# Performance work log

Hardware: AMD Instinct MI355X
Metric: run time of the kernel (lower is better)

The kernel has to match this reference:

```python
import jax, jax.numpy as jnp
import numpy as np

B, N, ND, H, FF, L, NH = 8, 200, 128, 256, 1024, 3, 8
DH = H // NH


def setup_inputs() -> dict:
    key = jax.random.key(0)
    ks = jax.random.split(key, 16)
    w = lambda k, s: jax.random.normal(k, s, jnp.float32) * 0.02
    return dict(
        h=jax.random.normal(ks[0], (B, N, ND), jnp.float32),
        xt=jax.random.uniform(ks[1], (B, N, N), jnp.float32),
        t=jax.random.uniform(ks[2], (B,), jnp.float32),
        tw1=w(ks[3], (1, H)), tb1=jnp.zeros(H), tw2=w(ks[4], (H, H)), tb2=jnp.zeros(H),
        ew=w(ks[5], (1, H)), eb=jnp.zeros(H),
        pw=w(ks[6], (ND, H)), pb=jnp.zeros(H),
        qkv_w=w(ks[7], (L, H, 3 * H)), qkv_b=jnp.zeros((L, 3 * H)),
        ao_w=w(ks[8], (L, H, H)), ao_b=jnp.zeros((L, H)),
        ln1_g=jnp.ones((L, H)), ln1_b=jnp.zeros((L, H)),
        f1_w=w(ks[9], (L, H, FF)), f1_b=jnp.zeros((L, FF)),
        f2_w=w(ks[10], (L, FF, H)), f2_b=jnp.zeros((L, H)),
        ln2_g=jnp.ones((L, H)), ln2_b=jnp.zeros((L, H)),
        ow1=w(ks[11], (3 * H, H)), ob1=jnp.zeros(H),
        ow2=w(ks[12], (H, 2)), ob2=jnp.zeros(2),
    )


def _ln(x, g, b, eps=1e-5):
    m = x.mean(-1, keepdims=True)
    v = x.var(-1, keepdims=True)
    return (x - m) / jnp.sqrt(v + eps) * g + b


def _forward(h, xt, t, tw1, tb1, tw2, tb2, ew, eb, pw, pb,
             qkv_w, qkv_b, ao_w, ao_b, ln1_g, ln1_b,
             f1_w, f1_b, f2_w, f2_b, ln2_g, ln2_b, ow1, ob1, ow2, ob2):
    b, n, _ = h.shape
    # time embedding: Linear -> SiLU -> Linear
    t_emb = jax.nn.silu(t[:, None] @ tw1 + tb1) @ tw2 + tb2          # (B,H)
    x = h @ pw + pb + t_emb[:, None, :]                               # (B,N,H)
    # post-norm TransformerEncoderLayer stack (ReLU FFN, eval mode)
    for l in range(L):
        qkv = x @ qkv_w[l] + qkv_b[l]
        q, k, v = jnp.split(qkv, 3, axis=-1)
        q = q.reshape(b, n, NH, DH)
        k = k.reshape(b, n, NH, DH)
        v = v.reshape(b, n, NH, DH)
        scores = jnp.einsum('bihd,bjhd->bhij', q, k) / np.sqrt(DH).astype(np.float32)
        attn = jax.nn.softmax(scores, axis=-1)
        o = jnp.einsum('bhij,bjhd->bihd', attn, v).reshape(b, n, H)
        o = o @ ao_w[l] + ao_b[l]
        x = _ln(x + o, ln1_g[l], ln1_b[l])
        f = jax.nn.relu(x @ f1_w[l] + f1_b[l]) @ f2_w[l] + f2_b[l]
        x = _ln(x + f, ln2_g[l], ln2_b[l])
    # edge head: concat([h_i, h_j, edge_emb]) @ W1 == sum of three partial matmuls
    edge_emb = xt[..., None] * ew[0] + eb                             # (B,N,N,H)
    wa, wb, wc = ow1[:H], ow1[H:2 * H], ow1[2 * H:]
    pre = (x @ wa)[:, :, None, :] + (x @ wb)[:, None, :, :] \
        + edge_emb @ wc + ob1                                         # (B,N,N,H)
    return jax.nn.silu(pre) @ ow2 + ob2                               # (B,N,N,2)


def reference(h, xt, t, tw1, tb1, tw2, tb2, ew, eb, pw, pb,
              qkv_w, qkv_b, ao_w, ao_b, ln1_g, ln1_b,
              f1_w, f1_b, f2_w, f2_b, ln2_g, ln2_b, ow1, ob1, ow2, ob2):
    return _forward(h, xt, t, tw1, tb1, tw2, tb2, ew, eb, pw, pb,
                    qkv_w, qkv_b, ao_w, ao_b, ln1_g, ln1_b,
                    f1_w, f1_b, f2_w, f2_b, ln2_g, ln2_b, ow1, ob1, ow2, ob2)
```

## Files before the change

### kernel.cpp

```cpp
#include <hip/hip_runtime.h>

#define Bdim 8
#define Nn 200
#define NDd 128
#define Hd 256
#define FFd 1024
#define Ld 3
#define NHh 8
#define DHd 32
#define Mtot (Bdim * Nn)
#define ZS 409600

typedef unsigned short u16;
typedef unsigned int u32;
using short8 = __attribute__((ext_vector_type(8))) short;
using fx4 = __attribute__((ext_vector_type(4))) float;

__device__ __forceinline__ float siluf(float x) {
  return x * __builtin_amdgcn_rcpf(1.0f + __expf(-x));
}

__device__ __forceinline__ void bsplit(float x, u16& h, u16& l) {
  u32 b = __float_as_uint(x);
  h = (u16)(b >> 16);
  float hf = __uint_as_float(b & 0xffff0000u);
  float r = x - hf;
  l = (u16)(__float_as_uint(r) >> 16);
}

__device__ __forceinline__ void store_xfrag(u16* __restrict__ xh,
                                            u16* __restrict__ xl, int m, int c,
                                            float v) {
  u32 o = ((u32)((m >> 4) * 8 + (c >> 5)) * 64 + ((c & 31) >> 3) * 16 +
           (m & 15)) * 8 + (c & 7);
  u16 hh, ll;
  bsplit(v, hh, ll);
  xh[o] = hh;
  xl[o] = ll;
}

struct SplitDesc {
  const float* s;
  u32 off;
  int K, N;
};
struct SplitArgs {
  SplitDesc d[14];
};

__global__ __launch_bounds__(256) void prep_kernel(
    SplitArgs a, u16* __restrict__ WH, u16* __restrict__ WL,
    const float* __restrict__ t, const float* __restrict__ tw1,
    const float* __restrict__ tb1, const float* __restrict__ tw2,
    const float* __restrict__ tb2, float* __restrict__ temb,
    const float* __restrict__ ew, const float* __restrict__ eb,
    const float* __restrict__ ow1, const float* __restrict__ ob1,
    float* __restrict__ u, float* __restrict__ w0) {
  __shared__ float s[Hd];
  if (blockIdx.y < 14) {
    SplitDesc dd = a.d[blockIdx.y];
    int idx = blockIdx.x * 256 + threadIdx.x;
    int total8 = dd.K * dd.N / 8;
    if (idx >= total8) return;
    int n = idx % dd.N;
    int kq = idx / dd.N;
    int ks = kq >> 2, q = kq & 3;
    int KS = dd.K >> 5;
    short8 vh, vl;
#pragma unroll
    for (int kr = 0; kr < 8; ++kr) {
      float v = dd.s[(size_t)(ks * 32 + q * 8 + kr) * dd.N + n];
      u16 hh, ll;
      bsplit(v, hh, ll);
      vh[kr] = (short)hh;
      vl[kr] = (short)ll;
    }
    u32 o = (((u32)(n >> 4) * KS + ks) * 64 + q * 16 + (n & 15)) * 8 + dd.off;
    *(short8*)(WH + o) = vh;
    *(short8*)(WL + o) = vl;
  } else {
    if (blockIdx.x < 8) {
      int b = blockIdx.x, h = threadIdx.x;
      float pre = t[b] * tw1[h] + tb1[h];
      s[h] = siluf(pre);
      __syncthreads();
      float acc = tb2[h];
#pragma unroll 8
      for (int k = 0; k < Hd; ++k) acc += s[k] * tw2[k * Hd + h];
      temb[b * Hd + h] = acc;
    } else if (blockIdx.x == 8) {
      int c = threadIdx.x;
      const float* wcp = ow1 + 2 * Hd * Hd;
      float uu = 0.f, ww = 0.f;
      for (int hh = 0; hh < Hd; ++hh) {
        float wv = wcp[hh * Hd + c];
        uu += ew[hh] * wv;
        ww += eb[hh] * wv;
      }
      u[c] = uu;
      w0[c] = ww + ob1[c];
    }
  }
}

__global__ __launch_bounds__(256) void proj_kernel(
    const float* __restrict__ h, const float* __restrict__ pw,
    const float* __restrict__ pb, const float* __restrict__ temb,
    float* __restrict__ x, u16* __restrict__ xh, u16* __restrict__ xl) {
  int m = blockIdx.x, n = threadIdx.x, b = m / Nn;
  __shared__ float hs[NDd];
  if (n < NDd) hs[n] = h[m * NDd + n];
  __syncthreads();
  float acc = pb[n] + temb[b * Hd + n];
#pragma unroll 8
  for (int k = 0; k < NDd; ++k) acc += hs[k] * pw[k * Hd + n];
  x[m * Hd + n] = acc;
  store_xfrag(xh, xl, m, n, acc);
}

template <int KSZ, int EPI, int MERGE>
__global__ __launch_bounds__(256) void mfma_gemm(
    const u16* __restrict__ ah, const u16* __restrict__ al,
    const float* __restrict__ pO, const float* __restrict__ pl,
    const u16* __restrict__ wh, const u16* __restrict__ wl,
    const float* __restrict__ bias, float* __restrict__ outf,
    u16* __restrict__ oh, u16* __restrict__ ol, int N, int KS,
    size_t zstride) {
  int lane = threadIdx.x & 63, wv = threadIdx.x >> 6;
  int rt = blockIdx.x * 4 + wv;
  int nt0 = blockIdx.y * 4;
  int ks0 = blockIdx.z * KSZ;
  int m16 = lane & 15, quad = lane >> 4;
  int mrow = rt * 16 + m16;
  int bq = mrow / Nn, iq = mrow % Nn;
  fx4 z4 = {0.f, 0.f, 0.f, 0.f};
  fx4 acc[4] = {z4, z4, z4, z4};
  const short8* pah = (const short8*)ah;
  const short8* pal = (const short8*)al;
  const short8* pwh = (const short8*)wh;
  const short8* pwl = (const short8*)wl;

  auto loadA = [&](int ks, short8& a_h, short8& a_l) {
    if (MERGE) {
      int head = ks0 + ks;
      float o8[8];
      float denom = 0.f;
#pragma unroll
      for (int z = 0; z < 4; ++z) {
        int base = ((bq * NHh + head) * 4 + z) * Nn + iq;
        denom += pl[base];
        const float* p = pO + (size_t)base * 32 + quad * 8;
        float4 v0 = *(const float4*)p;
        float4 v1 = *(const float4*)(p + 4);
        if (z == 0) {
          o8[0] = v0.x; o8[1] = v0.y; o8[2] = v0.z; o8[3] = v0.w;
          o8[4] = v1.x; o8[5] = v1.y; o8[6] = v1.z; o8[7] = v1.w;
        } else {
          o8[0] += v0.x; o8[1] += v0.y; o8[2] += v0.z; o8[3] += v0.w;
          o8[4] += v1.x; o8[5] += v1.y; o8[6] += v1.z; o8[7] += v1.w;
        }
      }
      float rd = 1.0f / denom;
#pragma unroll
      for (int e = 0; e < 8; ++e) {
        u16 hh, ll;
        bsplit(o8[e] * rd, hh, ll);
        a_h[e] = (short)hh;
        a_l[e] = (short)ll;
      }
    } else {
      a_h = pah[(size_t)(rt * KS + ks0 + ks) * 64 + lane];
      a_l = pal[(size_t)(rt * KS + ks0 + ks) * 64 + lane];
    }
  };

  short8 ca_h, ca_l, cb_h[4], cb_l[4];
  loadA(0, ca_h, ca_l);
#pragma unroll
  for (int nt = 0; nt < 4; ++nt) {
    size_t wi = ((size_t)(nt0 + nt) * KS + ks0) * 64 + lane;
    cb_h[nt] = pwh[wi];
    cb_l[nt] = pwl[wi];
  }
#pragma unroll
  for (int ks = 0; ks < KSZ; ++ks) {
    short8 na_h, na_l, nb_h[4], nb_l[4];
    if (ks + 1 < KSZ) {
      loadA(ks + 1, na_h, na_l);
#pragma unroll
      for (int nt = 0; nt < 4; ++nt) {
        size_t wi = ((size_t)(nt0 + nt) * KS + ks0 + ks + 1) * 64 + lane;
        nb_h[nt] = pwh[wi];
        nb_l[nt] = pwl[wi];
      }
    }
#pragma unroll
    for (int nt = 0; nt < 4; ++nt) {
      acc[nt] = __builtin_amdgcn_mfma_f32_16x16x32_bf16(ca_h, cb_h[nt], acc[nt], 0, 0, 0);
      acc[nt] = __builtin_amdgcn_mfma_f32_16x16x32_bf16(ca_h, cb_l[nt], acc[nt], 0, 0, 0);
      acc[nt] = __builtin_amdgcn_mfma_f32_16x16x32_bf16(ca_l, cb_h[nt], acc[nt], 0, 0, 0);
    }
    ca_h = na_h;
    ca_l = na_l;
#pragma unroll
    for (int nt = 0; nt < 4; ++nt) {
      cb_h[nt] = nb_h[nt];
      cb_l[nt] = nb_l[nt];
    }
  }

  size_t zoff = (size_t)blockIdx.z * zstride;
#pragma unroll
  for (int nt = 0; nt < 4; ++nt) {
    int col = (nt0 + nt) * 16 + m16;
    float bv = (bias && blockIdx.z == 0) ? bias[col] : 0.f;
#pragma unroll
    for (int r = 0; r < 4; ++r) {
      int row = rt * 16 + quad * 4 + r;
      float v = acc[nt][r] + bv;
      if (EPI == 0) {
        outf[zoff + (size_t)row * N + col] = v;
      } else {
        v = fmaxf(v, 0.f);
        u32 o = ((u32)(rt * 32 + (col >> 5)) * 64 + ((col & 31) >> 3) * 16 +
                 (row & 15)) * 8 + (col & 7);
        u16 hh, ll;
        bsplit(v, hh, ll);
        oh[o] = hh;
        ol[o] = ll;
      }
    }
  }
}

__global__ __launch_bounds__(256) void afbm_gemm(
    const u16* __restrict__ xh, const u16* __restrict__ xl,
    const u16* __restrict__ WHa, const u16* __restrict__ WLa,
    const u16* __restrict__ WHb, const u16* __restrict__ WLb,
    const float* __restrict__ w0, float* __restrict__ Af,
    float* __restrict__ Bm) {
  int lane = threadIdx.x & 63, wv = threadIdx.x >> 6;
  int rt = blockIdx.x * 4 + wv;
  int sel = blockIdx.y >> 2;
  int nt0 = (blockIdx.y & 3) * 4;
  const short8* pwh = (const short8*)(sel ? WHb : WHa);
  const short8* pwl = (const short8*)(sel ? WLb : WLa);
  float* outp = sel ? Bm : Af;
  fx4 z4 = {0.f, 0.f, 0.f, 0.f};
  fx4 acc[4] = {z4, z4, z4, z4};
  const short8* pah = (const short8*)xh + (size_t)(rt * 8) * 64 + lane;
  const short8* pal = (const short8*)xl + (size_t)(rt * 8) * 64 + lane;
#pragma unroll 4
  for (int ks = 0; ks < 8; ++ks) {
    short8 a_h = pah[ks * 64];
    short8 a_l = pal[ks * 64];
#pragma unroll
    for (int nt = 0; nt < 4; ++nt) {
      size_t wi = ((size_t)(nt0 + nt) * 8 + ks) * 64 + lane;
      short8 b_h = pwh[wi];
      short8 b_l = pwl[wi];
      acc[nt] = __builtin_amdgcn_mfma_f32_16x16x32_bf16(a_h, b_h, acc[nt], 0, 0, 0);
      acc[nt] = __builtin_amdgcn_mfma_f32_16x16x32_bf16(a_h, b_l, acc[nt], 0, 0, 0);
      acc[nt] = __builtin_amdgcn_mfma_f32_16x16x32_bf16(a_l, b_h, acc[nt], 0, 0, 0);
    }
  }
  int q = lane >> 4, n16 = lane & 15;
#pragma unroll
  for (int nt = 0; nt < 4; ++nt) {
    int col = (nt0 + nt) * 16 + n16;
    float bv = (sel == 0) ? w0[col] : 0.f;
#pragma unroll
    for (int r = 0; r < 4; ++r) {
      int row = rt * 16 + q * 4 + r;
      outp[(size_t)row * Hd + col] = acc[nt][r] + bv;
    }
  }
}

__global__ __launch_bounds__(256) void ln_res_kernel(
    float* __restrict__ x, const float* __restrict__ y, int ksplit,
    const float* __restrict__ bias, const float* __restrict__ g,
    const float* __restrict__ bb, u16* __restrict__ xh, u16* __restrict__ xl) {
  int m = blockIdx.x, tid = threadIdx.x;
  int lane = tid & 63, wid = tid >> 6;
  float v = x[m * Hd + tid] + bias[tid];
  for (int z = 0; z < ksplit; ++z)
    v += y[(size_t)z * ZS + m * Hd + tid];
  float s = v, s2 = v * v;
  for (int off = 32; off; off >>= 1) {
    s += __shfl_down(s, off);
    s2 += __shfl_down(s2, off);
  }
  __shared__ float ps[4], ps2[4];
  if (!lane) { ps[wid] = s; ps2[wid] = s2; }
  __syncthreads();
  float mean = (ps[0] + ps[1] + ps[2] + ps[3]) * (1.0f / Hd);
  float msq = (ps2[0] + ps2[1] + ps2[2] + ps2[3]) * (1.0f / Hd);
  float inv = rsqrtf(msq - mean * mean + 1e-5f);
  float o = (v - mean) * inv * g[tid] + bb[tid];
  x[m * Hd + tid] = o;
  store_xfrag(xh, xl, m, tid, o);
}

__global__ __launch_bounds__(256) void attn_flash(
    const float* __restrict__ qkv, float* __restrict__ pO,
    float* __restrict__ pl) {
  int jq = blockIdx.x, hd = blockIdx.y, b = blockIdx.z;
  int tid = threadIdx.x;
  __shared__ float Ks[50][32], Vs[50][32];
  for (int idx = tid; idx < 400; idx += 256) {
    int row = idx >> 3, c4 = (idx & 7) * 4;
    const float* src =
        qkv + ((size_t)(b * Nn + jq * 50 + row)) * (3 * Hd) + Hd + hd * DHd + c4;
    *(float4*)&Ks[row][c4] = *(const float4*)src;
    *(float4*)&Vs[row][c4] = *(const float4*)(src + Hd);
  }
  __syncthreads();
  if (tid >= Nn) return;
  int i = tid;
  float q[32];
  const float* qrow = qkv + ((size_t)(b * Nn + i)) * (3 * Hd) + hd * DHd;
#pragma unroll
  for (int c4 = 0; c4 < 32; c4 += 4)
    *(float4*)&q[c4] = *(const float4*)&qrow[c4];
  float O[32];
#pragma unroll
  for (int c = 0; c < 32; ++c) O[c] = 0.f;
  float l = 0.f;
#pragma unroll 2
  for (int j = 0; j < 50; ++j) {
    float kr[32], vr[32];
#pragma unroll
    for (int c4 = 0; c4 < 32; c4 += 4) {
      *(float4*)&kr[c4] = *(const float4*)&Ks[j][c4];
      *(float4*)&vr[c4] = *(const float4*)&Vs[j][c4];
    }
    float d = 0.f;
#pragma unroll
    for (int c = 0; c < 32; ++c) d += q[c] * kr[c];
    float p = __expf(d * 0.1767766952966369f);
    l += p;
#pragma unroll
    for (int c = 0; c < 32; ++c) O[c] += p * vr[c];
  }
  size_t base = (size_t)((b * NHh + hd) * 4 + jq) * Nn + i;
  pl[base] = l;
  float* po = pO + base * 32;
#pragma unroll
  for (int c4 = 0; c4 < 32; c4 += 4) *(float4*)&po[c4] = *(float4*)&O[c4];
}

__global__ __launch_bounds__(256) void final3_kernel(
    const float* __restrict__ Af, const float* __restrict__ Bm,
    const float* __restrict__ xt, const float* __restrict__ u,
    const float* __restrict__ ow2, const float* __restrict__ ob2,
    float* __restrict__ out) {
  int tid = threadIdx.x;
  int wid = tid >> 6, lane = tid & 63;
  int cg = lane & 31, jp = lane >> 5;
  int gw = blockIdx.x * 4 + wid;
  int bi = gw / 5;
  int jq = gw - bi * 5;
  int b = bi / Nn;

  float u8[8], w2[16], ar[8];
  *(float4*)&u8[0] = *(const float4*)&u[cg * 8];
  *(float4*)&u8[4] = *(const float4*)&u[cg * 8 + 4];
#pragma unroll
  for (int q = 0; q < 4; ++q)
    *(float4*)&w2[q * 4] = *(const float4*)&ow2[cg * 16 + q * 4];
  const float* arp = Af + (size_t)bi * Hd + cg * 8;
  *(float4*)&ar[0] = *(const float4*)&arp[0];
  *(float4*)&ar[4] = *(const float4*)&arp[4];
  float ob20 = ob2[0], ob21 = ob2[1];

  const float* xtrow = xt + (size_t)bi * Nn;
  const float* bmb = Bm + (size_t)(b * Nn) * Hd + cg * 8;
  for (int t = 0; t < 10; ++t) {
    int j0 = jq * 40 + t * 4;
    int jA = j0 + jp, jB = j0 + 2 + jp;
    float brA[8], brB[8];
    const float* pA = bmb + (size_t)jA * Hd;
    const float* pB = bmb + (size_t)jB * Hd;
    *(float4*)&brA[0] = *(const float4*)&pA[0];
    *(float4*)&brA[4] = *(const float4*)&pA[4];
    *(float4*)&brB[0] = *(const float4*)&pB[0];
    *(float4*)&brB[4] = *(const float4*)&pB[4];
    float xA = xtrow[jA], xB = xtrow[jB];
    float a0 = 0.f, a1 = 0.f, c0 = 0.f, c1 = 0.f;
#pragma unroll
    for (int c = 0; c < 8; ++c) {
      float preA = ar[c] + brA[c] + xA * u8[c];
      float sA = siluf(preA);
      a0 += sA * w2[2 * c];
      a1 += sA * w2[2 * c + 1];
      float preB = ar[c] + brB[c] + xB * u8[c];
      float sB = siluf(preB);
      c0 += sB * w2[2 * c];
      c1 += sB * w2[2 * c + 1];
    }
#pragma unroll
    for (int m = 1; m < 32; m <<= 1) {
      a0 += __shfl_xor(a0, m);
      a1 += __shfl_xor(a1, m);
      c0 += __shfl_xor(c0, m);
      c1 += __shfl_xor(c1, m);
    }
    if (cg == 0) {
      size_t pa = ((size_t)bi * Nn + jA) * 2;
      out[pa] = a0 + ob20;
      out[pa + 1] = a1 + ob21;
      size_t pb = ((size_t)bi * Nn + jB) * 2;
      out[pb] = c0 + ob20;
      out[pb + 1] = c1 + ob21;
    }
  }
}

extern "C" void kernel_launch(void* const* d_in, const int* in_sizes, int n_in,
                              void* d_out, int out_size, void* d_ws, size_t ws_size,
                              hipStream_t stream) {
  const float* h   = (const float*)d_in[0];
  const float* xt  = (const float*)d_in[1];
  const float* t   = (const float*)d_in[2];
  const float* tw1 = (const float*)d_in[3];
  const float* tb1 = (const float*)d_in[4];
  const float* tw2 = (const float*)d_in[5];
  const float* tb2 = (const float*)d_in[6];
  const float* ew  = (const float*)d_in[7];
  const float* eb  = (const float*)d_in[8];
  const float* pw  = (const float*)d_in[9];
  const float* pb  = (const float*)d_in[10];
  const float* qkv_w = (const float*)d_in[11];
  const float* qkv_b = (const float*)d_in[12];
  const float* ao_w  = (const float*)d_in[13];
  const float* ao_b  = (const float*)d_in[14];
  const float* ln1_g = (const float*)d_in[15];
  const float* ln1_b = (const float*)d_in[16];
  const float* f1_w  = (const float*)d_in[17];
  const float* f1_b  = (const float*)d_in[18];
  const float* f2_w  = (const float*)d_in[19];
  const float* f2_b  = (const float*)d_in[20];
  const float* ln2_g = (const float*)d_in[21];
  const float* ln2_b = (const float*)d_in[22];
  const float* ow1   = (const float*)d_in[23];
  const float* ob1   = (const float*)d_in[24];
  const float* ow2   = (const float*)d_in[25];
  const float* ob2   = (const float*)d_in[26];
  float* out = (float*)d_out;

  float* ws = (float*)d_ws;
  float* temb = ws;
  float* u    = ws + 2048;
  float* w0   = ws + 2304;
  float* x    = ws + 4096;
  u16*   x_h  = (u16*)(ws + 413696);
  u16*   x_l  = (u16*)(ws + 618496);
  float* qkvbuf = ws + 823296;
  float* aopart = ws + 823296;
  u16*   relu_h = (u16*)(ws + 823296);
  u16*   relu_l = (u16*)(ws + 1642496);
  float* Af     = ws + 823296;
  float* Bm     = ws + 1232896;
  float* pO_buf = ws + 2461696;
  float* f2part = ws + 2461696;
  float* pl_buf = ws + 4100096;
  u16*   WH   = (u16*)(ws + 4151296);
  u16*   WL   = (u16*)(ws + 5396480);

  const u32 QO = 0, AOO = 589824, F1O = 786432, F2O = 1572864,
            WAO = 2359296, WBO = 2424832;

  SplitArgs sa;
  for (int l = 0; l < Ld; ++l) {
    sa.d[l * 4 + 0] = {qkv_w + (size_t)l * 196608, QO + (u32)l * 196608, 256, 768};
    sa.d[l * 4 + 1] = {ao_w + (size_t)l * 65536, AOO + (u32)l * 65536, 256, 256};
    sa.d[l * 4 + 2] = {f1_w + (size_t)l * 262144, F1O + (u32)l * 262144, 256, 1024};
    sa.d[l * 4 + 3] = {f2_w + (size_t)l * 262144, F2O + (u32)l * 262144, 1024, 256};
  }
  sa.d[12] = {ow1, WAO, 256, 256};
  sa.d[13] = {ow1 + 65536, WBO, 256, 256};

  prep_kernel<<<dim3(128, 15), 256, 0, stream>>>(
      sa, WH, WL, t, tw1, tb1, tw2, tb2, temb, ew, eb, ow1, ob1, u, w0);
  proj_kernel<<<Mtot, 256, 0, stream>>>(h, pw, pb, temb, x, x_h, x_l);

  for (int l = 0; l < Ld; ++l) {
    mfma_gemm<8, 0, 0><<<dim3(25, 12, 1), 256, 0, stream>>>(
        x_h, x_l, nullptr, nullptr, WH + QO + (u32)l * 196608,
        WL + QO + (u32)l * 196608, qkv_b + l * 3 * Hd, qkvbuf, nullptr,
        nullptr, 3 * Hd, 8, 0);
    attn_flash<<<dim3(4, NHh, Bdim), 256, 0, stream>>>(qkvbuf, pO_buf, pl_buf);
    mfma_gemm<4, 0, 1><<<dim3(25, 4, 2), 256, 0, stream>>>(
        nullptr, nullptr, pO_buf, pl_buf, WH + AOO + (u32)l * 65536,
        WL + AOO + (u32)l * 65536, nullptr, aopart, nullptr, nullptr,
        Hd, 8, ZS);
    ln_res_kernel<<<Mtot, 256, 0, stream>>>(x, aopart, 2, ao_b + l * Hd,
                                            ln1_g + l * Hd, ln1_b + l * Hd,
                                            x_h, x_l);
    mfma_gemm<8, 1, 0><<<dim3(25, 16, 1), 256, 0, stream>>>(
        x_h, x_l, nullptr, nullptr, WH + F1O + (u32)l * 262144,
        WL + F1O + (u32)l * 262144, f1_b + l * FFd, nullptr, relu_h, relu_l,
        FFd, 8, 0);
    mfma_gemm<8, 0, 0><<<dim3(25, 4, 4), 256, 0, stream>>>(
        relu_h, relu_l, nullptr, nullptr, WH + F2O + (u32)l * 262144,
        WL + F2O + (u32)l * 262144, nullptr, f2part, nullptr, nullptr,
        Hd, 32, ZS);
    ln_res_kernel<<<Mtot, 256, 0, stream>>>(x, f2part, 4, f2_b + l * Hd,
                                            ln2_g + l * Hd, ln2_b + l * Hd,
                                            x_h, x_l);
  }

  afbm_gemm<<<dim3(25, 8), 256, 0, stream>>>(
      x_h, x_l, WH + WAO, WL + WAO, WH + WBO, WL + WBO, w0, Af, Bm);
  final3_kernel<<<2000, 256, 0, stream>>>(Af, Bm, xt, u, ow2, ob2, out);
}
```

Before: 374.1 us.

## Fold residual+LayerNorm into the following GEMM's A-operand load

Removes the standalone ln_res_kernel launches by computing residual sum, bias, and LayerNorm per 16-row strip inside a new gemm_lnfold kernel. The normalized rows go into shared memory and are split into bf16 hi/lo fragments on the fly as MFMA inputs. The LN result is written back as fp32 x by only one column block, using ping-pong xA/xB buffers. This saves launches and a global round trip of the bf16 fragments. In exchange, every column block redundantly recomputes LN for its strip, and the workspace layout is reorganized.

```diff
diff --git a/kernel.cpp b/kernel.cpp
--- a/kernel.cpp
+++ b/kernel.cpp
@@ -10,6 +10,7 @@
 #define DHd 32
 #define Mtot (Bdim * Nn)
 #define ZS 409600
+#define LNS 260
 
 typedef unsigned short u16;
 typedef unsigned int u32;
@@ -233,30 +234,95 @@
   }
 }
 
-__global__ __launch_bounds__(256) void afbm_gemm(
-    const u16* __restrict__ xh, const u16* __restrict__ xl,
-    const u16* __restrict__ WHa, const u16* __restrict__ WLa,
-    const u16* __restrict__ WHb, const u16* __restrict__ WLb,
-    const float* __restrict__ w0, float* __restrict__ Af,
-    float* __restrict__ Bm) {
-  int lane = threadIdx.x & 63, wv = threadIdx.x >> 6;
-  int rt = blockIdx.x * 4 + wv;
-  int sel = blockIdx.y >> 2;
-  int nt0 = (blockIdx.y & 3) * 4;
-  const short8* pwh = (const short8*)(sel ? WHb : WHa);
-  const short8* pwl = (const short8*)(sel ? WLb : WLa);
-  float* outp = sel ? Bm : Af;
+template <int NPARTS, int EPI, int BSEL>
+__global__ __launch_bounds__(256) void gemm_lnfold(
+    const float* __restrict__ xin, const float* __restrict__ parts,
+    const float* __restrict__ rbias, const float* __restrict__ g,
+    const float* __restrict__ bb, float* __restrict__ xout,
+    const u16* __restrict__ wh, const u16* __restrict__ wl,
+    const float* __restrict__ bias, float* __restrict__ outf,
+    u16* __restrict__ oh, u16* __restrict__ ol, int N,
+    int wsel, size_t osel) {
+  __shared__ float lnt[16][LNS];
+  int tid = threadIdx.x;
+  int lane = tid & 63, wv = tid >> 6;
+  int strip = blockIdx.x, by = blockIdx.y;
+
+  {
+    int row = tid >> 4;
+    int c0 = (tid & 15) * 16;
+    int grow = strip * 16 + row;
+    float v[16];
+    const float* xr = xin + (size_t)grow * Hd + c0;
+#pragma unroll
+    for (int e = 0; e < 16; e += 4) {
+      float4 xv = *(const float4*)(xr + e);
+      v[e] = xv.x; v[e + 1] = xv.y; v[e + 2] = xv.z; v[e + 3] = xv.w;
+    }
+#pragma unroll
+    for (int z = 0; z < NPARTS; ++z) {
+      const float* pr = parts + (size_t)z * ZS + (size_t)grow * Hd + c0;
+#pragma unroll
+      for (int e = 0; e < 16; e += 4) {
+        float4 pv = *(const float4*)(pr + e);
+        v[e] += pv.x; v[e + 1] += pv.y; v[e + 2] += pv.z; v[e + 3] += pv.w;
+      }
+    }
+    float s = 0.f, s2 = 0.f;
+#pragma unroll
+    for (int e = 0; e < 16; e += 4) {
+      float4 bv = *(const float4*)(rbias + c0 + e);
+      v[e] += bv.x; v[e + 1] += bv.y; v[e + 2] += bv.z; v[e + 3] += bv.w;
+#pragma unroll
+      for (int q = 0; q < 4; ++q) { s += v[e + q]; s2 += v[e + q] * v[e + q]; }
+    }
+#pragma unroll
+    for (int m = 1; m < 16; m <<= 1) {
+      s += __shfl_xor(s, m);
+      s2 += __shfl_xor(s2, m);
+    }
+    float mean = s * (1.0f / Hd);
+    float inv = rsqrtf(s2 * (1.0f / Hd) - mean * mean + 1e-5f);
+#pragma unroll
+    for (int e = 0; e < 16; e += 4) {
+      float4 gv = *(const float4*)(g + c0 + e);
+      float4 bbv = *(const float4*)(bb + c0 + e);
+      v[e] = (v[e] - mean) * inv * gv.x + bbv.x;
+      v[e + 1] = (v[e + 1] - mean) * inv * gv.y + bbv.y;
+      v[e + 2] = (v[e + 2] - mean) * inv * gv.z + bbv.z;
+      v[e + 3] = (v[e + 3] - mean) * inv * gv.w + bbv.w;
+      *(float4*)&lnt[row][c0 + e] = *(float4*)&v[e];
+    }
+    if (xout && by == 0) {
+      float* xo = xout + (size_t)grow * Hd + c0;
+#pragma unroll
+      for (int e = 0; e < 16; e += 4) *(float4*)(xo + e) = *(float4*)&v[e];
+    }
+  }
+  __syncthreads();
+
+  int m16 = lane & 15, quad = lane >> 4;
+  const short8* pwh = (const short8*)(BSEL ? wh + (size_t)by * wsel : wh);
+  const short8* pwl = (const short8*)(BSEL ? wl + (size_t)by * wsel : wl);
+  int ntbase = BSEL ? (wv * 4) : (by * 16 + wv * 4);
   fx4 z4 = {0.f, 0.f, 0.f, 0.f};
   fx4 acc[4] = {z4, z4, z4, z4};
-  const short8* pah = (const short8*)xh + (size_t)(rt * 8) * 64 + lane;
-  const short8* pal = (const short8*)xl + (size_t)(rt * 8) * 64 + lane;
-#pragma unroll 4
+#pragma unroll 2
   for (int ks = 0; ks < 8; ++ks) {
-    short8 a_h = pah[ks * 64];
-    short8 a_l = pal[ks * 64];
+    short8 a_h, a_l;
+    float4 a0 = *(const float4*)&lnt[m16][ks * 32 + quad * 8];
+    float4 a1 = *(const float4*)&lnt[m16][ks * 32 + quad * 8 + 4];
+    float av[8] = {a0.x, a0.y, a0.z, a0.w, a1.x, a1.y, a1.z, a1.w};
+#pragma unroll
+    for (int e = 0; e < 8; ++e) {
+      u16 hh, ll;
+      bsplit(av[e], hh, ll);
+      a_h[e] = (short)hh;
+      a_l[e] = (short)ll;
+    }
 #pragma unroll
     for (int nt = 0; nt < 4; ++nt) {
-      size_t wi = ((size_t)(nt0 + nt) * 8 + ks) * 64 + lane;
+      size_t wi = ((size_t)(ntbase + nt) * 8 + ks) * 64 + lane;
       short8 b_h = pwh[wi];
       short8 b_l = pwl[wi];
       acc[nt] = __builtin_amdgcn_mfma_f32_16x16x32_bf16(a_h, b_h, acc[nt], 0, 0, 0);
@@ -264,42 +330,36 @@
       acc[nt] = __builtin_amdgcn_mfma_f32_16x16x32_bf16(a_l, b_h, acc[nt], 0, 0, 0);
     }
   }
-  int q = lane >> 4, n16 = lane & 15;
+
+  float* outp = BSEL ? outf + (size_t)by * osel : outf;
 #pragma unroll
   for (int nt = 0; nt < 4; ++nt) {
-    int col = (nt0 + nt) * 16 + n16;
-    float bv = (sel == 0) ? w0[col] : 0.f;
+    int col = (ntbase + nt) * 16 + m16;
+    float bv = 0.f;
+    if (bias) {
+      if (BSEL) {
+        if (by == 0) bv = bias[col];
+      } else {
+        bv = bias[col];
+      }
+    }
 #pragma unroll
     for (int r = 0; r < 4; ++r) {
-      int row = rt * 16 + q * 4 + r;
-      outp[(size_t)row * Hd + col] = acc[nt][r] + bv;
-    }
-  }
-}
-
-__global__ __launch_bounds__(256) void ln_res_kernel(
-    float* __restrict__ x, const float* __restrict__ y, int ksplit,
-    const float* __restrict__ bias, const float* __restrict__ g,
-    const float* __restrict__ bb, u16* __restrict__ xh, u16* __restrict__ xl) {
-  int m = blockIdx.x, tid = threadIdx.x;
-  int lane = tid & 63, wid = tid >> 6;
-  float v = x[m * Hd + tid] + bias[tid];
-  for (int z = 0; z < ksplit; ++z)
-    v += y[(size_t)z * ZS + m * Hd + tid];
-  float s = v, s2 = v * v;
-  for (int off = 32; off; off >>= 1) {
-    s += __shfl_down(s, off);
-    s2 += __shfl_down(s2, off);
-  }
-  __shared__ float ps[4], ps2[4];
-  if (!lane) { ps[wid] = s; ps2[wid] = s2; }
-  __syncthreads();
-  float mean = (ps[0] + ps[1] + ps[2] + ps[3]) * (1.0f / Hd);
-  float msq = (ps2[0] + ps2[1] + ps2[2] + ps2[3]) * (1.0f / Hd);
-  float inv = rsqrtf(msq - mean * mean + 1e-5f);
-  float o = (v - mean) * inv * g[tid] + bb[tid];
-  x[m * Hd + tid] = o;
-  store_xfrag(xh, xl, m, tid, o);
+      int row = strip * 16 + quad * 4 + r;
+      float v = acc[nt][r] + bv;
+      if (EPI == 0) {
+        outp[(size_t)row * N + col] = v;
+      } else {
+        v = fmaxf(v, 0.f);
+        u32 o = ((u32)(strip * 32 + (col >> 5)) * 64 + ((col & 31) >> 3) * 16 +
+                 (row & 15)) * 8 + (col & 7);
+        u16 hh, ll;
+        bsplit(v, hh, ll);
+        oh[o] = hh;
+        ol[o] = ll;
+      }
+    }
+  }
 }
 
 __global__ __launch_bounds__(256) void attn_flash(
@@ -453,20 +513,21 @@
   float* temb = ws;
   float* u    = ws + 2048;
   float* w0   = ws + 2304;
-  float* x    = ws + 4096;
+  float* xA   = ws + 4096;
   u16*   x_h  = (u16*)(ws + 413696);
   u16*   x_l  = (u16*)(ws + 618496);
-  float* qkvbuf = ws + 823296;
-  float* aopart = ws + 823296;
-  u16*   relu_h = (u16*)(ws + 823296);
-  u16*   relu_l = (u16*)(ws + 1642496);
-  float* Af     = ws + 823296;
-  float* Bm     = ws + 1232896;
-  float* pO_buf = ws + 2461696;
-  float* f2part = ws + 2461696;
-  float* pl_buf = ws + 4100096;
-  u16*   WH   = (u16*)(ws + 4151296);
-  u16*   WL   = (u16*)(ws + 5396480);
+  float* xB   = ws + 823296;
+  float* qkvbuf = ws + 1232896;
+  float* aopart = ws + 2461696;
+  u16*   relu_h = (u16*)(ws + 3280896);
+  u16*   relu_l = (u16*)(ws + 4100096);
+  float* f2part = ws + 4919296;
+  float* pO_buf = ws + 6557696;
+  float* pl_buf = ws + 8196096;
+  u16*   WH   = (u16*)(ws + 8247296);
+  u16*   WL   = (u16*)(ws + 9492480);
+  float* Af   = qkvbuf;
+  float* Bm   = qkvbuf + ZS;
 
   const u32 QO = 0, AOO = 589824, F1O = 786432, F2O = 1572864,
             WAO = 2359296, WBO = 2424832;
@@ -483,35 +544,38 @@
 
   prep_kernel<<<dim3(128, 15), 256, 0, stream>>>(
       sa, WH, WL, t, tw1, tb1, tw2, tb2, temb, ew, eb, ow1, ob1, u, w0);
-  proj_kernel<<<Mtot, 256, 0, stream>>>(h, pw, pb, temb, x, x_h, x_l);
+  proj_kernel<<<Mtot, 256, 0, stream>>>(h, pw, pb, temb, xA, x_h, x_l);
 
   for (int l = 0; l < Ld; ++l) {
-    mfma_gemm<8, 0, 0><<<dim3(25, 12, 1), 256, 0, stream>>>(
-        x_h, x_l, nullptr, nullptr, WH + QO + (u32)l * 196608,
-        WL + QO + (u32)l * 196608, qkv_b + l * 3 * Hd, qkvbuf, nullptr,
-        nullptr, 3 * Hd, 8, 0);
+    if (l == 0) {
+      mfma_gemm<8, 0, 0><<<dim3(25, 12, 1), 256, 0, stream>>>(
+          x_h, x_l, nullptr, nullptr, WH + QO, WL + QO, qkv_b, qkvbuf,
+          nullptr, nullptr, 3 * Hd, 8, 0);
+    } else {
+      gemm_lnfold<4, 0, 0><<<dim3(100, 3), 256, 0, stream>>>(
+          xB, f2part, f2_b + (l - 1) * Hd, ln2_g + (l - 1) * Hd,
+          ln2_b + (l - 1) * Hd, xA, WH + QO + (u32)l * 196608,
+          WL + QO + (u32)l * 196608, qkv_b + l * 3 * Hd, qkvbuf, nullptr,
+          nullptr, 3 * Hd, 0, 0);
+    }
     attn_flash<<<dim3(4, NHh, Bdim), 256, 0, stream>>>(qkvbuf, pO_buf, pl_buf);
     mfma_gemm<4, 0, 1><<<dim3(25, 4, 2), 256, 0, stream>>>(
         nullptr, nullptr, pO_buf, pl_buf, WH + AOO + (u32)l * 65536,
         WL + AOO + (u32)l * 65536, nullptr, aopart, nullptr, nullptr,
         Hd, 8, ZS);
-    ln_res_kernel<<<Mtot, 256, 0, stream>>>(x, aopart, 2, ao_b + l * Hd,
-                                            ln1_g + l * Hd, ln1_b + l * Hd,
-                                            x_h, x_l);
-    mfma_gemm<8, 1, 0><<<dim3(25, 16, 1), 256, 0, stream>>>(
-        x_h, x_l, nullptr, nullptr, WH + F1O + (u32)l * 262144,
-        WL + F1O + (u32)l * 262144, f1_b + l * FFd, nullptr, relu_h, relu_l,
-        FFd, 8, 0);
+    gemm_lnfold<2, 1, 0><<<dim3(100, 4), 256, 0, stream>>>(
+        xA, aopart, ao_b + l * Hd, ln1_g + l * Hd, ln1_b + l * Hd, xB,
+        WH + F1O + (u32)l * 262144, WL + F1O + (u32)l * 262144,
+        f1_b + l * FFd, nullptr, relu_h, relu_l, FFd, 0, 0);
     mfma_gemm<8, 0, 0><<<dim3(25, 4, 4), 256, 0, stream>>>(
         relu_h, relu_l, nullptr, nullptr, WH + F2O + (u32)l * 262144,
         WL + F2O + (u32)l * 262144, nullptr, f2part, nullptr, nullptr,
         Hd, 32, ZS);
-    ln_res_kernel<<<Mtot, 256, 0, stream>>>(x, f2part, 4, f2_b + l * Hd,
-                                            ln2_g + l * Hd, ln2_b + l * Hd,
-                                            x_h, x_l);
-  }
-
-  afbm_gemm<<<dim3(25, 8), 256, 0, stream>>>(
-      x_h, x_l, WH + WAO, WL + WAO, WH + WBO, WL + WBO, w0, Af, Bm);
+  }
+
+  gemm_lnfold<4, 0, 1><<<dim3(100, 2), 256, 0, stream>>>(
+      xB, f2part, f2_b + 2 * Hd, ln2_g + 2 * Hd, ln2_b + 2 * Hd, nullptr,
+      WH + WAO, WL + WAO, w0, Af, nullptr, nullptr, Hd,
+      (int)(WBO - WAO), (size_t)ZS);
   final3_kernel<<<2000, 256, 0, stream>>>(Af, Bm, xt, u, ow2, ob2, out);
 }
```

Result: faster. 355.2 us, median of 2 (-5.1%).
